# Kernel tuning notes

Hardware: AMD Instinct MI355X
Metric: run time of the kernel (lower is better)

## Reference

```python
import jax, jax.numpy as jnp
import numpy as np

D = 1024
DQK = D // 8  # query/key projection dim

def setup_inputs() -> dict:
    key = jax.random.key(0)
    ks = jax.random.split(key, 8)
    B, N, M = 32, 1024, 1024
    s = 0.02
    return {
        "x": jax.random.normal(ks[0], (B, N, D), jnp.float32),
        "context": jax.random.normal(ks[1], (B, M, D), jnp.float32),
        "Wq": jax.random.normal(ks[2], (D, DQK), jnp.float32) * s,
        "bq": jnp.zeros((DQK,), jnp.float32),
        "Wk": jax.random.normal(ks[3], (D, DQK), jnp.float32) * s,
        "bk": jnp.zeros((DQK,), jnp.float32),
        "Wv": jax.random.normal(ks[4], (D, D), jnp.float32) * s,
        "bv": jnp.zeros((D,), jnp.float32),
    }

def reference(x, context, Wq, bq, Wk, bk, Wv, bv):
    # Linear projections (weights stored [in, out])
    Q = jnp.einsum("bnd,de->bne", x, Wq) + bq          # [B,N,DQK]
    K = jnp.einsum("bmd,de->bme", context, Wk) + bk    # [B,M,DQK]
    V = jnp.einsum("bmd,de->bme", context, Wv) + bv    # [B,M,D]
    # Unscaled attention scores (original has no 1/sqrt(d) factor)
    scores = jnp.einsum("bne,bme->bnm", Q, K)          # [B,N,M]
    weights = jax.nn.softmax(scores, axis=-1)          # [B,N,M]
    attended = jnp.einsum("bnm,bme->bne", weights, V)  # [B,N,D]
    return attended + x, weights
```

## Files before the change

### kernel.cpp

```cpp
#include <hip/hip_runtime.h>

using bf16   = __bf16;
using bf16x8 = __attribute__((ext_vector_type(8))) __bf16;
using f32x4  = __attribute__((ext_vector_type(4))) float;

constexpr int BATCH = 32;
constexpr int NQ    = 1024;
constexpr int MK    = 1024;
constexpr int DIM   = 1024;
constexpr int DQK   = 128;
constexpr int LP    = 40;

__global__ void transpose_split(const float* __restrict__ in, bf16* __restrict__ hiT,
                                bf16* __restrict__ loT, int R, int C) {
    int idx = blockIdx.x * 256 + threadIdx.x;
    if (idx >= R * C) return;
    int r = idx / C, c = idx - r * C;
    float v = in[idx];
    bf16 h = (bf16)v;
    hiT[(size_t)c * R + r] = h;
    loT[(size_t)c * R + r] = (bf16)(v - (float)h);
}

__global__ void transpose_cvt(const float* __restrict__ in, bf16* __restrict__ outT,
                              int R, int C) {
    int idx = blockIdx.x * 256 + threadIdx.x;
    if (idx >= R * C) return;
    int r = idx / C, c = idx - r * C;
    outT[(size_t)c * R + r] = (bf16)in[idx];
}

__global__ __launch_bounds__(256) void gemm_bt_split(const float* __restrict__ A,
                                                     const bf16* __restrict__ BhT,
                                                     const bf16* __restrict__ BlT,
                                                     const float* __restrict__ bias,
                                                     bf16* __restrict__ Chi,
                                                     bf16* __restrict__ Clo,
                                                     int M, int N, int K) {
    __shared__ alignas(16) bf16 Ah[64 * LP];
    __shared__ alignas(16) bf16 Al[64 * LP];
    __shared__ alignas(16) bf16 Bh[64 * LP];
    __shared__ alignas(16) bf16 Bl[64 * LP];
    const int tid = threadIdx.x;
    const int wv = tid >> 6, ln = tid & 63, q = ln >> 4, l16 = ln & 15;
    const int m0 = blockIdx.x * 64, n0 = blockIdx.y * 64;
    const int sr = tid >> 2, sc = (tid & 3) * 8;

    f32x4 acc[4] = {{0,0,0,0},{0,0,0,0},{0,0,0,0},{0,0,0,0}};

    for (int k0 = 0; k0 < K; k0 += 32) {
        const float* ap = A + (size_t)(m0 + sr) * K + k0 + sc;
        f32x4 a0 = *reinterpret_cast<const f32x4*>(ap);
        f32x4 a1 = *reinterpret_cast<const f32x4*>(ap + 4);
        bf16x8 hv, lv;
#pragma unroll
        for (int e = 0; e < 8; ++e) {
            float v = (e < 4) ? a0[e] : a1[e - 4];
            bf16 h = (bf16)v;
            hv[e] = h;
            lv[e] = (bf16)(v - (float)h);
        }
        *reinterpret_cast<bf16x8*>(&Ah[sr * LP + sc]) = hv;
        *reinterpret_cast<bf16x8*>(&Al[sr * LP + sc]) = lv;
        *reinterpret_cast<bf16x8*>(&Bh[sr * LP + sc]) =
            *reinterpret_cast<const bf16x8*>(BhT + (size_t)(n0 + sr) * K + k0 + sc);
        *reinterpret_cast<bf16x8*>(&Bl[sr * LP + sc]) =
            *reinterpret_cast<const bf16x8*>(BlT + (size_t)(n0 + sr) * K + k0 + sc);
        __syncthreads();
        bf16x8 afh = *reinterpret_cast<const bf16x8*>(&Ah[(wv * 16 + l16) * LP + q * 8]);
        bf16x8 afl = *reinterpret_cast<const bf16x8*>(&Al[(wv * 16 + l16) * LP + q * 8]);
#pragma unroll
        for (int t = 0; t < 4; ++t) {
            bf16x8 bfh = *reinterpret_cast<const bf16x8*>(&Bh[(t * 16 + l16) * LP + q * 8]);
            bf16x8 bfl = *reinterpret_cast<const bf16x8*>(&Bl[(t * 16 + l16) * LP + q * 8]);
            acc[t] = __builtin_amdgcn_mfma_f32_16x16x32_bf16(afh, bfh, acc[t], 0, 0, 0);
            acc[t] = __builtin_amdgcn_mfma_f32_16x16x32_bf16(afh, bfl, acc[t], 0, 0, 0);
            acc[t] = __builtin_amdgcn_mfma_f32_16x16x32_bf16(afl, bfh, acc[t], 0, 0, 0);
        }
        __syncthreads();
    }
#pragma unroll
    for (int t = 0; t < 4; ++t) {
        const int col = n0 + t * 16 + l16;
        const float bb = bias[col];
#pragma unroll
        for (int r = 0; r < 4; ++r) {
            const int row = m0 + wv * 16 + q * 4 + r;
            float v = acc[t][r] + bb;
            bf16 h = (bf16)v;
            Chi[(size_t)row * N + col] = h;
            Clo[(size_t)row * N + col] = (bf16)(v - (float)h);
        }
    }
}

__global__ __launch_bounds__(256) void gemm_bt_plain(const float* __restrict__ A,
                                                     const bf16* __restrict__ BT,
                                                     const float* __restrict__ bias,
                                                     bf16* __restrict__ C,
                                                     int M, int N, int K) {
    __shared__ alignas(16) bf16 Ah[64 * LP];
    __shared__ alignas(16) bf16 Bh[64 * LP];
    const int tid = threadIdx.x;
    const int wv = tid >> 6, ln = tid & 63, q = ln >> 4, l16 = ln & 15;
    const int m0 = blockIdx.x * 64, n0 = blockIdx.y * 64;
    const int sr = tid >> 2, sc = (tid & 3) * 8;

    f32x4 acc[4] = {{0,0,0,0},{0,0,0,0},{0,0,0,0},{0,0,0,0}};

    for (int k0 = 0; k0 < K; k0 += 32) {
        const float* ap = A + (size_t)(m0 + sr) * K + k0 + sc;
        f32x4 a0 = *reinterpret_cast<const f32x4*>(ap);
        f32x4 a1 = *reinterpret_cast<const f32x4*>(ap + 4);
        bf16x8 hv;
#pragma unroll
        for (int e = 0; e < 8; ++e) hv[e] = (bf16)((e < 4) ? a0[e] : a1[e - 4]);
        *reinterpret_cast<bf16x8*>(&Ah[sr * LP + sc]) = hv;
        *reinterpret_cast<bf16x8*>(&Bh[sr * LP + sc]) =
            *reinterpret_cast<const bf16x8*>(BT + (size_t)(n0 + sr) * K + k0 + sc);
        __syncthreads();
        bf16x8 af = *reinterpret_cast<const bf16x8*>(&Ah[(wv * 16 + l16) * LP + q * 8]);
#pragma unroll
        for (int t = 0; t < 4; ++t) {
            bf16x8 bf = *reinterpret_cast<const bf16x8*>(&Bh[(t * 16 + l16) * LP + q * 8]);
            acc[t] = __builtin_amdgcn_mfma_f32_16x16x32_bf16(af, bf, acc[t], 0, 0, 0);
        }
        __syncthreads();
    }
#pragma unroll
    for (int t = 0; t < 4; ++t) {
        const int col = n0 + t * 16 + l16;
        const float bb = bias[col];
#pragma unroll
        for (int r = 0; r < 4; ++r) {
            const int row = m0 + wv * 16 + q * 4 + r;
            C[(size_t)row * N + col] = (bf16)(acc[t][r] + bb);
        }
    }
}

__global__ __launch_bounds__(256) void scores_softmax(const bf16* __restrict__ Qh,
                                                      const bf16* __restrict__ Ql,
                                                      const bf16* __restrict__ Kh,
                                                      const bf16* __restrict__ Kl,
                                                      float* __restrict__ Wout) {
    __shared__ alignas(16) bf16 Qhs[16 * 136];
    __shared__ alignas(16) bf16 Qls[16 * 136];
    __shared__ float redm[4][16];
    __shared__ float reds[4][16];

    const int tid = threadIdx.x;
    const int wv = tid >> 6, ln = tid & 63, q = ln >> 4, l16 = ln & 15;
    const int nb = blockIdx.x;
    const int b  = blockIdx.y;

    {
        int r = tid >> 4, c = (tid & 15) * 8;
        size_t g = ((size_t)(b * NQ + nb * 16 + r)) * DQK + c;
        *reinterpret_cast<bf16x8*>(&Qhs[r * 136 + c]) = *reinterpret_cast<const bf16x8*>(Qh + g);
        *reinterpret_cast<bf16x8*>(&Qls[r * 136 + c]) = *reinterpret_cast<const bf16x8*>(Ql + g);
    }
    __syncthreads();

    const bf16* Khb = Kh + (size_t)b * MK * DQK;
    const bf16* Klb = Kl + (size_t)b * MK * DQK;

    f32x4 accs[16];
#pragma unroll
    for (int i = 0; i < 16; ++i) accs[i] = (f32x4){0, 0, 0, 0};

#pragma unroll
    for (int i = 0; i < 16; ++i) {
        const int ct = wv * 16 + i;
        const size_t krow = (size_t)(ct * 16 + l16) * DQK;
#pragma unroll
        for (int kk = 0; kk < 4; ++kk) {
            bf16x8 afh = *reinterpret_cast<const bf16x8*>(&Qhs[l16 * 136 + kk * 32 + q * 8]);
            bf16x8 afl = *reinterpret_cast<const bf16x8*>(&Qls[l16 * 136 + kk * 32 + q * 8]);
            bf16x8 bfh = *reinterpret_cast<const bf16x8*>(Khb + krow + kk * 32 + q * 8);
            bf16x8 bfl = *reinterpret_cast<const bf16x8*>(Klb + krow + kk * 32 + q * 8);
            accs[i] = __builtin_amdgcn_mfma_f32_16x16x32_bf16(afh, bfh, accs[i], 0, 0, 0);
            accs[i] = __builtin_amdgcn_mfma_f32_16x16x32_bf16(afh, bfl, accs[i], 0, 0, 0);
            accs[i] = __builtin_amdgcn_mfma_f32_16x16x32_bf16(afl, bfh, accs[i], 0, 0, 0);
        }
    }

    float mx[4], sm[4];
#pragma unroll
    for (int r = 0; r < 4; ++r) {
        float m = accs[0][r];
#pragma unroll
        for (int i = 1; i < 16; ++i) m = fmaxf(m, accs[i][r]);
#pragma unroll
        for (int off = 1; off < 16; off <<= 1) m = fmaxf(m, __shfl_xor(m, off, 64));
        mx[r] = m;
    }
    if (l16 == 0) {
#pragma unroll
        for (int r = 0; r < 4; ++r) redm[wv][q * 4 + r] = mx[r];
    }
    __syncthreads();
#pragma unroll
    for (int r = 0; r < 4; ++r) {
        float m = redm[0][q * 4 + r];
#pragma unroll
        for (int w = 1; w < 4; ++w) m = fmaxf(m, redm[w][q * 4 + r]);
        mx[r] = m;
        sm[r] = 0.f;
    }
#pragma unroll
    for (int i = 0; i < 16; ++i)
#pragma unroll
        for (int r = 0; r < 4; ++r) {
            float e = __expf(accs[i][r] - mx[r]);
            accs[i][r] = e;
            sm[r] += e;
        }
#pragma unroll
    for (int r = 0; r < 4; ++r) {
        float s = sm[r];
#pragma unroll
        for (int off = 1; off < 16; off <<= 1) s += __shfl_xor(s, off, 64);
        sm[r] = s;
    }
    if (l16 == 0) {
#pragma unroll
        for (int r = 0; r < 4; ++r) reds[wv][q * 4 + r] = sm[r];
    }
    __syncthreads();
    float inv[4];
#pragma unroll
    for (int r = 0; r < 4; ++r) {
        float s = reds[0][q * 4 + r] + reds[1][q * 4 + r] + reds[2][q * 4 + r] + reds[3][q * 4 + r];
        inv[r] = 1.f / s;
    }
    const size_t rowbase = (size_t)b * NQ + nb * 16;
#pragma unroll
    for (int i = 0; i < 16; ++i) {
        const int col = (wv * 16 + i) * 16 + l16;
#pragma unroll
        for (int r = 0; r < 4; ++r)
            Wout[(rowbase + q * 4 + r) * MK + col] = accs[i][r] * inv[r];
    }
}

__global__ __launch_bounds__(256) void attn_out(const float* __restrict__ W,
                                                const bf16* __restrict__ V,
                                                const float* __restrict__ X,
                                                float* __restrict__ Out) {
    __shared__ alignas(16) bf16 Al[64 * LP];
    __shared__ alignas(16) bf16 Bl[64 * LP];
    const int tid = threadIdx.x;
    const int wv = tid >> 6, ln = tid & 63, q = ln >> 4, l16 = ln & 15;
    const int b = blockIdx.z;
    const size_t bo = (size_t)b << 20;
    const int m0 = blockIdx.x * 64;
    const int n0 = blockIdx.y * 64;
    const int ar = tid >> 2, ac = (tid & 3) * 8;
    const int bk = tid >> 3, bn = (tid & 7) * 8;

    f32x4 acc[4] = {{0,0,0,0},{0,0,0,0},{0,0,0,0},{0,0,0,0}};

    for (int k0 = 0; k0 < MK; k0 += 32) {
        const float* wp = W + bo + (size_t)(m0 + ar) * MK + k0 + ac;
        f32x4 w0 = *reinterpret_cast<const f32x4*>(wp);
        f32x4 w1 = *reinterpret_cast<const f32x4*>(wp + 4);
        bf16x8 wv8;
#pragma unroll
        for (int e = 0; e < 8; ++e) wv8[e] = (bf16)((e < 4) ? w0[e] : w1[e - 4]);
        *reinterpret_cast<bf16x8*>(&Al[ar * LP + ac]) = wv8;
        bf16x8 v8 = *reinterpret_cast<const bf16x8*>(V + bo + (size_t)(k0 + bk) * DIM + n0 + bn);
#pragma unroll
        for (int e = 0; e < 8; ++e) Bl[(bn + e) * LP + bk] = v8[e];
        __syncthreads();
        bf16x8 af = *reinterpret_cast<const bf16x8*>(&Al[(wv * 16 + l16) * LP + q * 8]);
#pragma unroll
        for (int t = 0; t < 4; ++t) {
            bf16x8 bf = *reinterpret_cast<const bf16x8*>(&Bl[(t * 16 + l16) * LP + q * 8]);
            acc[t] = __builtin_amdgcn_mfma_f32_16x16x32_bf16(af, bf, acc[t], 0, 0, 0);
        }
        __syncthreads();
    }
#pragma unroll
    for (int t = 0; t < 4; ++t) {
        const int col = n0 + t * 16 + l16;
#pragma unroll
        for (int r = 0; r < 4; ++r) {
            const int row = m0 + wv * 16 + q * 4 + r;
            const size_t idx = bo + (size_t)row * DIM + col;
            Out[idx] = acc[t][r] + X[idx];
        }
    }
}

extern "C" void kernel_launch(void* const* d_in, const int* in_sizes, int n_in,
                              void* d_out, int out_size, void* d_ws, size_t ws_size,
                              hipStream_t stream) {
    const float* x   = (const float*)d_in[0];
    const float* ctx = (const float*)d_in[1];
    const float* Wq  = (const float*)d_in[2];
    const float* bq  = (const float*)d_in[3];
    const float* Wk  = (const float*)d_in[4];
    const float* bk  = (const float*)d_in[5];
    const float* Wv  = (const float*)d_in[6];
    const float* bv  = (const float*)d_in[7];

    float* out0 = (float*)d_out;
    float* out1 = out0 + (size_t)BATCH * NQ * DIM;

    bf16* wqTh = (bf16*)d_ws;
    bf16* wqTl = wqTh + (size_t)DQK * DIM;
    bf16* wkTh = wqTl + (size_t)DQK * DIM;
    bf16* wkTl = wkTh + (size_t)DQK * DIM;
    bf16* wvT  = wkTl + (size_t)DQK * DIM;
    bf16* Qhi  = wvT  + (size_t)DIM * DIM;
    bf16* Qlo  = Qhi  + (size_t)BATCH * NQ * DQK;
    bf16* Khi  = Qlo  + (size_t)BATCH * NQ * DQK;
    bf16* Klo  = Khi  + (size_t)BATCH * MK * DQK;
    bf16* Vs   = Klo  + (size_t)BATCH * MK * DQK;

    transpose_split<<<(DIM * DQK + 255) / 256, 256, 0, stream>>>(Wq, wqTh, wqTl, DIM, DQK);
    transpose_split<<<(DIM * DQK + 255) / 256, 256, 0, stream>>>(Wk, wkTh, wkTl, DIM, DQK);
    transpose_cvt<<<(DIM * DIM + 255) / 256, 256, 0, stream>>>(Wv, wvT, DIM, DIM);

    gemm_bt_split<<<dim3((BATCH * NQ) / 64, DQK / 64), 256, 0, stream>>>(
        x, wqTh, wqTl, bq, Qhi, Qlo, BATCH * NQ, DQK, DIM);
    gemm_bt_split<<<dim3((BATCH * MK) / 64, DQK / 64), 256, 0, stream>>>(
        ctx, wkTh, wkTl, bk, Khi, Klo, BATCH * MK, DQK, DIM);
    gemm_bt_plain<<<dim3((BATCH * MK) / 64, DIM / 64), 256, 0, stream>>>(
        ctx, wvT, bv, Vs, BATCH * MK, DIM, DIM);

    scores_softmax<<<dim3(NQ / 16, BATCH), 256, 0, stream>>>(Qhi, Qlo, Khi, Klo, out1);

    attn_out<<<dim3(NQ / 64, DIM / 64, BATCH), 256, 0, stream>>>(out1, Vs, x, out0);
}
```

Baseline: 1.254 ms.

## Use 128x128 MFMA tiles with direct-to-LDS loads for V projection and attention output

Replaces the 64x64 V-projection and attention-output GEMMs with 128x128 block tiles, where each wave computes 4x4 MFMA fragments. Operands are staged in bf16 and fetched into LDS with global_load_lds. Context is pre-converted to bf16, V is produced transposed so both GEMMs read K-contiguous operands, and softmax writes a bf16 copy of the weights for the final GEMM. This removes per-tile fp32→bf16 conversion and the scalar transposed LDS stores, and raises data reuse per tile. The cost is extra workspace traffic: a bf16 copy of context and a bf16 copy of the weights.

```diff
diff --git a/kernel.cpp b/kernel.cpp
--- a/kernel.cpp
+++ b/kernel.cpp
@@ -10,6 +10,22 @@
 constexpr int DIM   = 1024;
 constexpr int DQK   = 128;
 constexpr int LP    = 40;
+
+__device__ __forceinline__ void gll16(const bf16* g, bf16* l) {
+    __builtin_amdgcn_global_load_lds((const __attribute__((address_space(1))) void*)g,
+                                     (__attribute__((address_space(3))) void*)l, 16, 0, 0);
+}
+
+__global__ void cvt_bf16(const float* __restrict__ in, bf16* __restrict__ out, int n) {
+    int i = (blockIdx.x * 256 + threadIdx.x) * 8;
+    if (i >= n) return;
+    f32x4 a = *reinterpret_cast<const f32x4*>(in + i);
+    f32x4 b = *reinterpret_cast<const f32x4*>(in + i + 4);
+    bf16x8 o;
+#pragma unroll
+    for (int e = 0; e < 4; ++e) { o[e] = (bf16)a[e]; o[e + 4] = (bf16)b[e]; }
+    *reinterpret_cast<bf16x8*>(out + i) = o;
+}
 
 __global__ void transpose_split(const float* __restrict__ in, bf16* __restrict__ hiT,
                                 bf16* __restrict__ loT, int R, int C) {
@@ -94,56 +110,117 @@
     }
 }
 
-__global__ __launch_bounds__(256) void gemm_bt_plain(const float* __restrict__ A,
-                                                     const bf16* __restrict__ BT,
-                                                     const float* __restrict__ bias,
-                                                     bf16* __restrict__ C,
-                                                     int M, int N, int K) {
-    __shared__ alignas(16) bf16 Ah[64 * LP];
-    __shared__ alignas(16) bf16 Bh[64 * LP];
+__global__ __launch_bounds__(256) void vproj_vt(const bf16* __restrict__ Aw,
+                                                const bf16* __restrict__ Bc,
+                                                const float* __restrict__ bv,
+                                                bf16* __restrict__ VT) {
+    __shared__ alignas(16) bf16 At[128 * 32];
+    __shared__ alignas(16) bf16 Bt[128 * 32];
     const int tid = threadIdx.x;
-    const int wv = tid >> 6, ln = tid & 63, q = ln >> 4, l16 = ln & 15;
-    const int m0 = blockIdx.x * 64, n0 = blockIdx.y * 64;
-    const int sr = tid >> 2, sc = (tid & 3) * 8;
-
-    f32x4 acc[4] = {{0,0,0,0},{0,0,0,0},{0,0,0,0},{0,0,0,0}};
-
-    for (int k0 = 0; k0 < K; k0 += 32) {
-        const float* ap = A + (size_t)(m0 + sr) * K + k0 + sc;
-        f32x4 a0 = *reinterpret_cast<const f32x4*>(ap);
-        f32x4 a1 = *reinterpret_cast<const f32x4*>(ap + 4);
-        bf16x8 hv;
-#pragma unroll
-        for (int e = 0; e < 8; ++e) hv[e] = (bf16)((e < 4) ? a0[e] : a1[e - 4]);
-        *reinterpret_cast<bf16x8*>(&Ah[sr * LP + sc]) = hv;
-        *reinterpret_cast<bf16x8*>(&Bh[sr * LP + sc]) =
-            *reinterpret_cast<const bf16x8*>(BT + (size_t)(n0 + sr) * K + k0 + sc);
-        __syncthreads();
-        bf16x8 af = *reinterpret_cast<const bf16x8*>(&Ah[(wv * 16 + l16) * LP + q * 8]);
-#pragma unroll
-        for (int t = 0; t < 4; ++t) {
-            bf16x8 bf = *reinterpret_cast<const bf16x8*>(&Bh[(t * 16 + l16) * LP + q * 8]);
-            acc[t] = __builtin_amdgcn_mfma_f32_16x16x32_bf16(af, bf, acc[t], 0, 0, 0);
-        }
-        __syncthreads();
-    }
-#pragma unroll
-    for (int t = 0; t < 4; ++t) {
-        const int col = n0 + t * 16 + l16;
-        const float bb = bias[col];
+    const int w = tid >> 6, ln = tid & 63, q = ln >> 4, l16 = ln & 15;
+    const int wm = w >> 1, wn = w & 1;
+    const int m0 = blockIdx.x * 128;
+    const int n0 = blockIdx.y * 128;
+    const int lrow = ln >> 2, lk = (ln & 3) * 8;
+
+    f32x4 acc[4][4] = {};
+
+    for (int k0 = 0; k0 < DIM; k0 += 32) {
+#pragma unroll
+        for (int j = 0; j < 2; ++j) {
+            const int row = (w * 2 + j) * 16 + lrow;
+            gll16(Aw + (size_t)(m0 + row) * DIM + k0 + lk, &At[(w * 2 + j) * 512]);
+            gll16(Bc + (size_t)(n0 + row) * DIM + k0 + lk, &Bt[(w * 2 + j) * 512]);
+        }
+        __syncthreads();
+        bf16x8 af[4], bfr[4];
+#pragma unroll
+        for (int i = 0; i < 4; ++i)
+            af[i] = *reinterpret_cast<const bf16x8*>(&At[(wm * 64 + i * 16 + l16) * 32 + q * 8]);
+#pragma unroll
+        for (int j = 0; j < 4; ++j)
+            bfr[j] = *reinterpret_cast<const bf16x8*>(&Bt[(wn * 64 + j * 16 + l16) * 32 + q * 8]);
+#pragma unroll
+        for (int i = 0; i < 4; ++i)
+#pragma unroll
+            for (int j = 0; j < 4; ++j)
+                acc[i][j] = __builtin_amdgcn_mfma_f32_16x16x32_bf16(af[i], bfr[j], acc[i][j], 0, 0, 0);
+        __syncthreads();
+    }
+#pragma unroll
+    for (int i = 0; i < 4; ++i)
 #pragma unroll
         for (int r = 0; r < 4; ++r) {
-            const int row = m0 + wv * 16 + q * 4 + r;
-            C[(size_t)row * N + col] = (bf16)(acc[t][r] + bb);
-        }
-    }
+            const int row = m0 + wm * 64 + i * 16 + q * 4 + r;
+            const float bb = bv[row];
+#pragma unroll
+            for (int j = 0; j < 4; ++j) {
+                const int col = n0 + wn * 64 + j * 16 + l16;
+                VT[(size_t)row * (BATCH * MK) + col] = (bf16)(acc[i][j][r] + bb);
+            }
+        }
+}
+
+__global__ __launch_bounds__(256) void attn_out_128(const bf16* __restrict__ Wbf,
+                                                    const bf16* __restrict__ VT,
+                                                    const float* __restrict__ X,
+                                                    float* __restrict__ Out) {
+    __shared__ alignas(16) bf16 At[128 * 32];
+    __shared__ alignas(16) bf16 Bt[128 * 32];
+    const int tid = threadIdx.x;
+    const int w = tid >> 6, ln = tid & 63, q = ln >> 4, l16 = ln & 15;
+    const int wm = w >> 1, wn = w & 1;
+    const int mb = blockIdx.x;
+    const int m0 = mb * 128;
+    const int n0 = blockIdx.y * 128;
+    const int b  = mb >> 3;
+    const int lrow = ln >> 2, lk = (ln & 3) * 8;
+    const bf16* Bb = VT + (size_t)b * MK;
+
+    f32x4 acc[4][4] = {};
+
+    for (int k0 = 0; k0 < MK; k0 += 32) {
+#pragma unroll
+        for (int j = 0; j < 2; ++j) {
+            const int row = (w * 2 + j) * 16 + lrow;
+            gll16(Wbf + (size_t)(m0 + row) * MK + k0 + lk, &At[(w * 2 + j) * 512]);
+            gll16(Bb + (size_t)(n0 + row) * (BATCH * MK) + k0 + lk, &Bt[(w * 2 + j) * 512]);
+        }
+        __syncthreads();
+        bf16x8 af[4], bfr[4];
+#pragma unroll
+        for (int i = 0; i < 4; ++i)
+            af[i] = *reinterpret_cast<const bf16x8*>(&At[(wm * 64 + i * 16 + l16) * 32 + q * 8]);
+#pragma unroll
+        for (int j = 0; j < 4; ++j)
+            bfr[j] = *reinterpret_cast<const bf16x8*>(&Bt[(wn * 64 + j * 16 + l16) * 32 + q * 8]);
+#pragma unroll
+        for (int i = 0; i < 4; ++i)
+#pragma unroll
+            for (int j = 0; j < 4; ++j)
+                acc[i][j] = __builtin_amdgcn_mfma_f32_16x16x32_bf16(af[i], bfr[j], acc[i][j], 0, 0, 0);
+        __syncthreads();
+    }
+#pragma unroll
+    for (int i = 0; i < 4; ++i)
+#pragma unroll
+        for (int j = 0; j < 4; ++j) {
+            const int col = n0 + wn * 64 + j * 16 + l16;
+#pragma unroll
+            for (int r = 0; r < 4; ++r) {
+                const int row = m0 + wm * 64 + i * 16 + q * 4 + r;
+                const size_t idx = (size_t)row * DIM + col;
+                Out[idx] = acc[i][j][r] + X[idx];
+            }
+        }
 }
 
 __global__ __launch_bounds__(256) void scores_softmax(const bf16* __restrict__ Qh,
                                                       const bf16* __restrict__ Ql,
                                                       const bf16* __restrict__ Kh,
                                                       const bf16* __restrict__ Kl,
-                                                      float* __restrict__ Wout) {
+                                                      float* __restrict__ Wout,
+                                                      bf16* __restrict__ Wbf) {
     __shared__ alignas(16) bf16 Qhs[16 * 136];
     __shared__ alignas(16) bf16 Qls[16 * 136];
     __shared__ float redm[4][16];
@@ -204,7 +281,7 @@
     for (int r = 0; r < 4; ++r) {
         float m = redm[0][q * 4 + r];
 #pragma unroll
-        for (int w = 1; w < 4; ++w) m = fmaxf(m, redm[w][q * 4 + r]);
+        for (int wq = 1; wq < 4; ++wq) m = fmaxf(m, redm[wq][q * 4 + r]);
         mx[r] = m;
         sm[r] = 0.f;
     }
@@ -230,65 +307,19 @@
     __syncthreads();
     float inv[4];
 #pragma unroll
-    for (int r = 0; r < 4; ++r) {
-        float s = reds[0][q * 4 + r] + reds[1][q * 4 + r] + reds[2][q * 4 + r] + reds[3][q * 4 + r];
-        inv[r] = 1.f / s;
-    }
+    for (int r = 0; r < 4; ++r)
+        inv[r] = 1.f / (reds[0][q * 4 + r] + reds[1][q * 4 + r] +
+                        reds[2][q * 4 + r] + reds[3][q * 4 + r]);
     const size_t rowbase = (size_t)b * NQ + nb * 16;
 #pragma unroll
     for (int i = 0; i < 16; ++i) {
         const int col = (wv * 16 + i) * 16 + l16;
 #pragma unroll
-        for (int r = 0; r < 4; ++r)
-            Wout[(rowbase + q * 4 + r) * MK + col] = accs[i][r] * inv[r];
-    }
-}
-
-__global__ __launch_bounds__(256) void attn_out(const float* __restrict__ W,
-                                                const bf16* __restrict__ V,
-                                                const float* __restrict__ X,
-                                                float* __restrict__ Out) {
-    __shared__ alignas(16) bf16 Al[64 * LP];
-    __shared__ alignas(16) bf16 Bl[64 * LP];
-    const int tid = threadIdx.x;
-    const int wv = tid >> 6, ln = tid & 63, q = ln >> 4, l16 = ln & 15;
-    const int b = blockIdx.z;
-    const size_t bo = (size_t)b << 20;
-    const int m0 = blockIdx.x * 64;
-    const int n0 = blockIdx.y * 64;
-    const int ar = tid >> 2, ac = (tid & 3) * 8;
-    const int bk = tid >> 3, bn = (tid & 7) * 8;
-
-    f32x4 acc[4] = {{0,0,0,0},{0,0,0,0},{0,0,0,0},{0,0,0,0}};
-
-    for (int k0 = 0; k0 < MK; k0 += 32) {
-        const float* wp = W + bo + (size_t)(m0 + ar) * MK + k0 + ac;
-        f32x4 w0 = *reinterpret_cast<const f32x4*>(wp);
-        f32x4 w1 = *reinterpret_cast<const f32x4*>(wp + 4);
-        bf16x8 wv8;
-#pragma unroll
-        for (int e = 0; e < 8; ++e) wv8[e] = (bf16)((e < 4) ? w0[e] : w1[e - 4]);
-        *reinterpret_cast<bf16x8*>(&Al[ar * LP + ac]) = wv8;
-        bf16x8 v8 = *reinterpret_cast<const bf16x8*>(V + bo + (size_t)(k0 + bk) * DIM + n0 + bn);
-#pragma unroll
-        for (int e = 0; e < 8; ++e) Bl[(bn + e) * LP + bk] = v8[e];
-        __syncthreads();
-        bf16x8 af = *reinterpret_cast<const bf16x8*>(&Al[(wv * 16 + l16) * LP + q * 8]);
-#pragma unroll
-        for (int t = 0; t < 4; ++t) {
-            bf16x8 bf = *reinterpret_cast<const bf16x8*>(&Bl[(t * 16 + l16) * LP + q * 8]);
-            acc[t] = __builtin_amdgcn_mfma_f32_16x16x32_bf16(af, bf, acc[t], 0, 0, 0);
-        }
-        __syncthreads();
-    }
-#pragma unroll
-    for (int t = 0; t < 4; ++t) {
-        const int col = n0 + t * 16 + l16;
-#pragma unroll
         for (int r = 0; r < 4; ++r) {
-            const int row = m0 + wv * 16 + q * 4 + r;
-            const size_t idx = bo + (size_t)row * DIM + col;
-            Out[idx] = acc[t][r] + X[idx];
+            const float v = accs[i][r] * inv[r];
+            const size_t idx = (rowbase + q * 4 + r) * MK + col;
+            Wout[idx] = v;
+            Wbf[idx]  = (bf16)v;
         }
     }
 }
@@ -317,20 +348,24 @@
     bf16* Qlo  = Qhi  + (size_t)BATCH * NQ * DQK;
     bf16* Khi  = Qlo  + (size_t)BATCH * NQ * DQK;
     bf16* Klo  = Khi  + (size_t)BATCH * MK * DQK;
-    bf16* Vs   = Klo  + (size_t)BATCH * MK * DQK;
+    bf16* VT   = Klo  + (size_t)BATCH * MK * DQK;
+    bf16* ctxb = VT   + (size_t)DIM * BATCH * MK;
+    bf16* Wbf  = ctxb + (size_t)BATCH * MK * DIM;
 
     transpose_split<<<(DIM * DQK + 255) / 256, 256, 0, stream>>>(Wq, wqTh, wqTl, DIM, DQK);
     transpose_split<<<(DIM * DQK + 255) / 256, 256, 0, stream>>>(Wk, wkTh, wkTl, DIM, DQK);
     transpose_cvt<<<(DIM * DIM + 255) / 256, 256, 0, stream>>>(Wv, wvT, DIM, DIM);
+    cvt_bf16<<<(BATCH * MK * DIM / 8 + 255) / 256, 256, 0, stream>>>(
+        ctx, ctxb, BATCH * MK * DIM);
 
     gemm_bt_split<<<dim3((BATCH * NQ) / 64, DQK / 64), 256, 0, stream>>>(
         x, wqTh, wqTl, bq, Qhi, Qlo, BATCH * NQ, DQK, DIM);
     gemm_bt_split<<<dim3((BATCH * MK) / 64, DQK / 64), 256, 0, stream>>>(
         ctx, wkTh, wkTl, bk, Khi, Klo, BATCH * MK, DQK, DIM);
-    gemm_bt_plain<<<dim3((BATCH * MK) / 64, DIM / 64), 256, 0, stream>>>(
-        ctx, wvT, bv, Vs, BATCH * MK, DIM, DIM);
-
-    scores_softmax<<<dim3(NQ / 16, BATCH), 256, 0, stream>>>(Qhi, Qlo, Khi, Klo, out1);
-
-    attn_out<<<dim3(NQ / 64, DIM / 64, BATCH), 256, 0, stream>>>(out1, Vs, x, out0);
-}
+
+    vproj_vt<<<dim3(DIM / 128, (BATCH * MK) / 128), 256, 0, stream>>>(wvT, ctxb, bv, VT);
+
+    scores_softmax<<<dim3(NQ / 16, BATCH), 256, 0, stream>>>(Qhi, Qlo, Khi, Klo, out1, Wbf);
+
+    attn_out_128<<<dim3((BATCH * NQ) / 128, DIM / 128), 256, 0, stream>>>(Wbf, VT, x, out0);
+}
```

Result: faster. 1.010 ms (-19.5%).
